# Performance work log

Measured on AMD Instinct MI355X. Metric: run time of the kernel, lower is better.

## Reference

```python
import jax, jax.numpy as jnp
import numpy as np

Q = 9          # D2Q9
G = 8          # dihedral group of the square
X = YD = 768   # spatial grid
HID = 32       # tau_net hidden width
N_IN = 6       # moments with order <= 2 (indices 0..5, contiguous by construction)
LOWER_TAU = 0.8


def _build_stencil():
    # D2Q9 velocities and weights
    e = np.array([[0, 0], [1, 0], [0, 1], [-1, 0], [0, -1],
                  [1, 1], [-1, 1], [-1, -1], [1, -1]], dtype=np.float64)
    w = np.array([4 / 9] + [1 / 9] * 4 + [1 / 36] * 4, dtype=np.float64)
    # natural moment matrix: rows are monomials ex^px * ey^py, ordered so that
    # moment_order = [0,1,1,2,2,2,3,3,4]  ->  in_indices=[0..5], out_indices=[6,7,8]
    exps = [(0, 0), (1, 0), (0, 1), (2, 0), (1, 1), (0, 2), (2, 1), (1, 2), (2, 2)]
    M = np.stack([e[:, 0] ** px * e[:, 1] ** py for px, py in exps])  # [Q, Q]
    Minv = np.linalg.inv(M)
    # symmetry group of the square: 4 rotations x {id, x-axis reflection}
    rots = [np.array([[np.cos(a), -np.sin(a)], [np.sin(a), np.cos(a)]])
            for a in (0.0, np.pi / 2, np.pi, 3 * np.pi / 2)]
    refl = np.array([[1.0, 0.0], [0.0, -1.0]])
    Rs = rots + [r @ refl for r in rots]
    perms = []
    for R in Rs:
        Re = np.rint(e @ R.T)
        P = np.zeros((Q, Q))
        for i in range(Q):
            j = int(np.where((e == Re[i]).all(axis=1))[0][0])
            P[j, i] = 1.0  # velocity i maps to velocity j under R
        perms.append(P)
    P = np.stack(perms)                                   # [G, Q, Q]
    actions = np.einsum('qp,gpr,rs->gqs', M, P, Minv)      # moment action  M P M^-1
    Pt = P.transpose(0, 2, 1)                              # P^-1 = P^T
    inv_actions = np.einsum('qp,gpr,rs->gqs', M, Pt, Minv)
    return (M.astype(np.float32), Minv.astype(np.float32),
            actions.astype(np.float32), inv_actions.astype(np.float32),
            e.astype(np.float32), w.astype(np.float32))


def setup_inputs() -> dict:
    key = jax.random.key(0)
    kf, k1, k2, k3 = jax.random.split(key, 4)
    M, Minv, actions, inv_actions, e, w = _build_stencil()
    f = jax.random.uniform(kf, (Q, X, YD), dtype=jnp.float32)
    s = 0.1
    return {
        'f': f,
        'M': jnp.asarray(M), 'Minv': jnp.asarray(Minv),
        'actions': jnp.asarray(actions), 'inv_actions': jnp.asarray(inv_actions),
        'e': jnp.asarray(e), 'w': jnp.asarray(w),
        'W1': jax.random.normal(k1, (N_IN, HID), jnp.float32) * s,
        'b1': jnp.zeros((HID,), jnp.float32),
        'W2': jax.random.normal(k2, (HID, HID), jnp.float32) * s,
        'b2': jnp.zeros((HID,), jnp.float32),
        'W3': jax.random.normal(k3, (HID, Q - N_IN), jnp.float32) * s,
        'b3': jnp.zeros((Q - N_IN,), jnp.float32),
    }


def reference(f, M, Minv, actions, inv_actions, e, w, W1, b1, W2, b2, W3, b3):
    # --- moment transform: m = M f, moved to channel-last [X, Y, Q] ---
    m = jnp.einsum('qp,pxy->xyq', M, f)
    # --- equivariant tau net on low-order moments ---
    x_in = m[..., :N_IN]                                   # in_indices = 0..5
    Ainv = inv_actions[:, :N_IN, :N_IN]                    # [G, 6, 6]
    A = actions[:, N_IN:, N_IN:]                           # [G, 3, 3] (out_indices)
    xg = jnp.einsum('gij,xyj->gxyi', Ainv, x_in)           # [G, X, Y, 6]
    h = jax.nn.relu(xg @ W1 + b1)
    h = jax.nn.relu(h @ W2 + b2)
    o = h @ W3 + b3                                        # [G, X, Y, 3]
    out = jnp.einsum('gij,gxyj->xyi', A, o)                # sum over group -> [X, Y, 3]
    tau_hi = 1.5 + jax.nn.elu(out)                         # gt_half: > 0.5
    taus = jnp.full(m.shape, LOWER_TAU, m.dtype).at[..., N_IN:].set(tau_hi)
    # --- equilibrium moments: meq = M feq(rho, u) (quadratic BGK, cs^2=1/3) ---
    rho = m[..., 0:1]                                      # natural moments: m0=rho
    u = m[..., 1:3] / rho                                  # m1,m2 = momentum
    eu = jnp.einsum('qd,xyd->xyq', e, u)
    usq = jnp.sum(u * u, axis=-1, keepdims=True)
    feq = w * rho * (1.0 + 3.0 * eu + 4.5 * eu * eu - 1.5 * usq)
    meq = jnp.einsum('qp,xyp->xyq', M, feq)
    # --- MRT collision + inverse transform ---
    m_post = m - (m - meq) / taus
    return jnp.einsum('pq,xyq->pxy', Minv, m_post)
```

## Files before the change

### kernel.cpp

```cpp
#include <hip/hip_runtime.h>
#include <hip/hip_bf16.h>
#include <math.h>

#define Q 9
#define NPIX (768 * 768)

typedef short bf16x8 __attribute__((ext_vector_type(8)));
typedef short s16x2 __attribute__((ext_vector_type(2)));
typedef float f32x4 __attribute__((ext_vector_type(4)));
typedef int i32x4 __attribute__((ext_vector_type(4)));

#define A1BV 512
#define A3V  1024
#define A2V  1536
#define B3TF 6656

__device__ __forceinline__ unsigned short f2bf(float x) {
    unsigned u = __builtin_bit_cast(unsigned, x);
    unsigned r = u + 0x7FFFu + ((u >> 16) & 1u);
    return (unsigned short)(r >> 16);
}

__device__ __forceinline__ unsigned pk2(float e, float o) {
    __hip_bfloat162 h = __float22bfloat162_rn(make_float2(e, o));
    unsigned u;
    __builtin_memcpy(&u, &h, 4);
    return u;
}

__device__ __forceinline__ unsigned relu2(unsigned d) {
    s16x2 v = __builtin_bit_cast(s16x2, d);
    const s16x2 z = {0, 0};
    v = __builtin_elementwise_max(v, z);
    return __builtin_bit_cast(unsigned, v);
}

__device__ __forceinline__ bf16x8 mk8(unsigned w0, unsigned w1, unsigned w2, unsigned w3) {
    i32x4 t = {(int)w0, (int)w1, (int)w2, (int)w3};
    return __builtin_bit_cast(bf16x8, t);
}

__global__ void prep_kernel(const float* __restrict__ actions,
                            const float* __restrict__ inv_actions,
                            const float* __restrict__ W1,
                            const float* __restrict__ b1,
                            const float* __restrict__ W2,
                            const float* __restrict__ W3,
                            const float* __restrict__ b3,
                            short* __restrict__ wsb,
                            float* __restrict__ wsf) {
    const int idx = blockIdx.x * 256 + threadIdx.x;
    if (idx < 8192) {
        int j = idx & 7, l = (idx >> 3) & 63, g = (idx >> 9) & 7, half = idx >> 12;
        int m = l & 15, quad = l >> 4, k = quad * 8 + j;
        int feat = 8 * (m >> 2) + (m & 3) + 4 * half;
        float v = 0.f;
        if (k < 6) {
            #pragma unroll
            for (int i = 0; i < 6; i++)
                v += inv_actions[g * 81 + i * 9 + k] * W1[i * 32 + feat];
        } else if (k == 6) v = b1[feat];
        wsb[idx] = (short)f2bf(v);
    } else if (idx < 12288) {
        int t = idx - 8192;
        int j = t & 7, l = (t >> 3) & 63, g = t >> 9;
        int m = l & 15, quad = l >> 4, k = quad * 8 + j;
        float v = 0.f;
        if (m < 3) {
            #pragma unroll
            for (int j3 = 0; j3 < 3; j3++)
                v += W3[k * 3 + j3] * actions[g * 81 + (6 + m) * 9 + (6 + j3)];
        }
        wsb[idx] = (short)f2bf(v);
    } else if (idx < 13312) {
        int t = idx - 12288;
        int j = t & 7, l = (t >> 3) & 63, half = t >> 9;
        int m = l & 15, quad = l >> 4, k = quad * 8 + j;
        int feat = 8 * (m >> 2) + (m & 3) + 4 * half;
        wsb[idx] = (short)f2bf(W2[k * 32 + feat]);
    } else if (idx < 13315) {
        int t = idx - 13312;
        float acc = 0.f;
        for (int g = 0; g < 8; g++)
            #pragma unroll
            for (int j = 0; j < 3; j++)
                acc += actions[g * 81 + (6 + t) * 9 + (6 + j)] * b3[j];
        wsf[B3TF + t] = acc;
    }
}

__global__ __launch_bounds__(256, 4) void lbm_kernel(
    const float* __restrict__ f,
    const float* __restrict__ Minv,
    const float* __restrict__ w,
    const float* __restrict__ b2,
    const short* __restrict__ wsb,
    const float* __restrict__ wsf,
    float* __restrict__ out) {
    __shared__ float oL[4][64][4];
    (void)Minv;
    (void)w;

    const int tid = threadIdx.x;
    const int wv = tid >> 6;
    const int l = tid & 63;
    const int quad = l >> 4;
    const int lc = l & 15;
    const int p = blockIdx.x * 256 + tid;

    float fv0 = f[0 * NPIX + p], fv1 = f[1 * NPIX + p], fv2 = f[2 * NPIX + p];
    float fv3 = f[3 * NPIX + p], fv4 = f[4 * NPIX + p], fv5 = f[5 * NPIX + p];
    float fv6 = f[6 * NPIX + p], fv7 = f[7 * NPIX + p], fv8 = f[8 * NPIX + p];
    float sa = fv5 + fv6, sb = fv7 + fv8, sc = fv5 - fv6, sd = fv7 - fv8;
    float sab = sa + sb;
    float m4 = sc + sd;
    float p13 = fv1 + fv3, d13 = fv1 - fv3, p24 = fv2 + fv4, d24 = fv2 - fv4;
    float m0 = fv0 + p13 + p24 + sab;
    float m1 = d13 + (sc - sd);
    float m2 = d24 + (sa - sb);
    float m3 = p13 + sab;
    float m5 = p24 + sab;

    unsigned mp0 = pk2(m0, m1), mp1 = pk2(m2, m3), mp2 = pk2(m4, m5);
    const unsigned CONE = 0x00003F80u;
    bf16x8 B1[4];
    #pragma unroll
    for (int nb = 0; nb < 4; nb++) {
        int src = ((nb << 4) | lc) << 2;
        unsigned a = (unsigned)__builtin_amdgcn_ds_bpermute(src, (int)mp0);
        unsigned b = (unsigned)__builtin_amdgcn_ds_bpermute(src, (int)mp1);
        unsigned c = (unsigned)__builtin_amdgcn_ds_bpermute(src, (int)mp2);
        B1[nb] = mk8(a, b, c, CONE);
    }

    const bf16x8* wsv = (const bf16x8*)wsb;
    bf16x8 a2a = wsv[A2V + l], a2b = wsv[A2V + 64 + l];
    f32x4 c2iA = *(const f32x4*)(b2 + 8 * quad);
    f32x4 c2iB = *(const f32x4*)(b2 + 8 * quad + 4);
    float b30 = wsf[B3TF + 0], b31 = wsf[B3TF + 1], b32 = wsf[B3TF + 2];
    f32x4 oinit;
    oinit[0] = (quad == 0) ? b30 : 0.f;
    oinit[1] = (quad == 0) ? b31 : 0.f;
    oinit[2] = (quad == 0) ? b32 : 0.f;
    oinit[3] = 0.f;
    f32x4 oacc[4] = {oinit, oinit, oinit, oinit};

    bf16x8 a1a = wsv[l], a1b = wsv[A1BV + l], a3 = wsv[A3V + l];

    #pragma unroll 1
    for (int g = 0; g < 8; g++) {
        const int gn = (g + 1) & 7;
        bf16x8 na1a = wsv[gn * 64 + l];
        bf16x8 na1b = wsv[A1BV + gn * 64 + l];
        bf16x8 na3  = wsv[A3V + gn * 64 + l];
        #pragma unroll
        for (int nb = 0; nb < 4; nb++) {
            f32x4 z = {0.f, 0.f, 0.f, 0.f};
            f32x4 c1a = __builtin_amdgcn_mfma_f32_16x16x32_bf16(a1a, B1[nb], z, 0, 0, 0);
            f32x4 c1b = __builtin_amdgcn_mfma_f32_16x16x32_bf16(a1b, B1[nb], z, 0, 0, 0);
            bf16x8 B2 = mk8(
                relu2(pk2(c1a[0], c1a[1])),
                relu2(pk2(c1a[2], c1a[3])),
                relu2(pk2(c1b[0], c1b[1])),
                relu2(pk2(c1b[2], c1b[3])));
            f32x4 c2a = __builtin_amdgcn_mfma_f32_16x16x32_bf16(a2a, B2, c2iA, 0, 0, 0);
            f32x4 c2b = __builtin_amdgcn_mfma_f32_16x16x32_bf16(a2b, B2, c2iB, 0, 0, 0);
            bf16x8 B3 = mk8(
                relu2(pk2(c2a[0], c2a[1])),
                relu2(pk2(c2a[2], c2a[3])),
                relu2(pk2(c2b[0], c2b[1])),
                relu2(pk2(c2b[2], c2b[3])));
            oacc[nb] = __builtin_amdgcn_mfma_f32_16x16x32_bf16(a3, B3, oacc[nb], 0, 0, 0);
        }
        a1a = na1a; a1b = na1b; a3 = na3;
    }

    if (quad == 0) {
        #pragma unroll
        for (int nb = 0; nb < 4; nb++)
            *(f32x4*)&oL[wv][nb * 16 + lc][0] = oacc[nb];
    }
    f32x4 ov = *(const f32x4*)&oL[wv][l][0];

    int p2 = p;
    asm("" : "+v"(p2));
    float fr0 = f[0 * NPIX + p2], fr1 = f[1 * NPIX + p2], fr2 = f[2 * NPIX + p2];
    float fr3 = f[3 * NPIX + p2], fr4 = f[4 * NPIX + p2], fr5 = f[5 * NPIX + p2];
    float fr6 = f[6 * NPIX + p2], fr7 = f[7 * NPIX + p2], fr8 = f[8 * NPIX + p2];

    float tinv[3];
    #pragma unroll
    for (int i = 0; i < 3; i++) {
        float o = ov[i];
        float el = (o > 0.f) ? o : (__expf(o) - 1.f);
        tinv[i] = __builtin_amdgcn_rcpf(1.5f + el);
    }

    float rho = m0;
    float ir = __builtin_amdgcn_rcpf(rho);
    float ux = m1 * ir, uy = m2 * ir;
    float usq = ux * ux + uy * uy;
    float base = 1.f - 1.5f * usq;
    float w1r = rho * (1.f / 9.f), w5r = rho * (1.f / 36.f);
    float bx = 3.f * ux, ax = fmaf(4.5f * ux, ux, base);
    float feq1 = w1r * (ax + bx), feq3 = w1r * (ax - bx);
    float by = 3.f * uy, ay = fmaf(4.5f * uy, uy, base);
    float feq2 = w1r * (ay + by), feq4 = w1r * (ay - by);
    float ss = ux + uy, bs = 3.f * ss, as_ = fmaf(4.5f * ss, ss, base);
    float feq5 = w5r * (as_ + bs), feq7 = w5r * (as_ - bs);
    float dd = uy - ux, bd = 3.f * dd, ad = fmaf(4.5f * dd, dd, base);
    float feq6 = w5r * (ad + bd), feq8 = w5r * (ad - bd);

    float g1 = fr1 - feq1, g2 = fr2 - feq2, g3 = fr3 - feq3, g4 = fr4 - feq4;
    float g5 = fr5 - feq5, g6 = fr6 - feq6, g7 = fr7 - feq7, g8 = fr8 - feq8;
    float pa = g1 + g3, pb = g2 + g4;
    float ea = g5 + g6, eb = g7 + g8, ec = g5 - g6, ed = g7 - g8;
    float eab = ea + eb;
    float m3p = pa + eab, m5p = pb + eab, m8p = eab;
    float m6p = ea - eb, m4p = ec + ed, m7p = ec - ed;

    float d3 = 1.25f * m3p, h3 = 0.625f * m3p;
    float d5 = 1.25f * m5p, h5 = 0.625f * m5p;
    float k4 = 0.3125f * m4p;
    float h6 = (0.5f * tinv[0]) * m6p, k6 = 0.5f * h6;
    float h7 = (0.5f * tinv[1]) * m7p, k7 = 0.5f * h7;
    float d8 = tinv[2] * m8p, h8 = 0.5f * d8, k8 = 0.5f * h8;

    float c0 = d8 - d3 - d5;
    float c1 = h3 - h7 - h8;
    float c2 = h5 - h6 - h8;
    float c3 = h3 + h7 - h8;
    float c4 = h5 + h6 - h8;
    float sA = k4 + k7, sB = k6 + k8, sC = k4 + k8;
    float sD = k6 + k7, sE = k7 + k8, sF = k4 + k6;
    float c5 = sA + sB, c6 = sB - sA, c7 = sC - sD, c8 = sE - sF;

    __builtin_nontemporal_store(fr0 - c0, &out[0 * NPIX + p]);
    __builtin_nontemporal_store(fr1 - c1, &out[1 * NPIX + p]);
    __builtin_nontemporal_store(fr2 - c2, &out[2 * NPIX + p]);
    __builtin_nontemporal_store(fr3 - c3, &out[3 * NPIX + p]);
    __builtin_nontemporal_store(fr4 - c4, &out[4 * NPIX + p]);
    __builtin_nontemporal_store(fr5 - c5, &out[5 * NPIX + p]);
    __builtin_nontemporal_store(fr6 - c6, &out[6 * NPIX + p]);
    __builtin_nontemporal_store(fr7 - c7, &out[7 * NPIX + p]);
    __builtin_nontemporal_store(fr8 - c8, &out[8 * NPIX + p]);
}

extern "C" void kernel_launch(void* const* d_in, const int* in_sizes, int n_in,
                              void* d_out, int out_size, void* d_ws, size_t ws_size,
                              hipStream_t stream) {
    const float* f           = (const float*)d_in[0];
    const float* Minv        = (const float*)d_in[2];
    const float* actions     = (const float*)d_in[3];
    const float* inv_actions = (const float*)d_in[4];
    const float* w           = (const float*)d_in[6];
    const float* W1          = (const float*)d_in[7];
    const float* b1          = (const float*)d_in[8];
    const float* W2          = (const float*)d_in[9];
    const float* b2          = (const float*)d_in[10];
    const float* W3          = (const float*)d_in[11];
    const float* b3          = (const float*)d_in[12];
    float* outp = (float*)d_out;
    short* wsb = (short*)d_ws;
    float* wsf = (float*)d_ws;

    prep_kernel<<<53, 256, 0, stream>>>(actions, inv_actions, W1, b1, W2, W3, b3, wsb, wsf);
    lbm_kernel<<<NPIX / 256, 256, 0, stream>>>(f, Minv, w, b2, wsb, wsf, outp);
}
```

Measured before the change: 121.1 us.

## Switch MLP to 32x32x16 MFMA tiles and peel last group iteration

Rewrites the per-group MLP to use 32x32x16 bf16 MFMAs over 32-pixel tiles instead of 16x16x32 over 16-pixel blocks. The weights are repacked in the prep kernel with a hidden-unit permutation so the MFMA output layout feeds directly into the next layer's B operand. This cuts the instruction count and the bpermute shuffles. The final group iteration is peeled so the reload of f overlaps with MFMA work. Occupancy is lowered to 3 blocks per SM to make room for the larger accumulators, which risks reduced latency hiding.

New measurement: 119.5 us. Within noise of the previous version (-1.3%).

```diff
diff --git a/kernel.cpp b/kernel.cpp
--- a/kernel.cpp
+++ b/kernel.cpp
@@ -8,12 +8,18 @@
 typedef short bf16x8 __attribute__((ext_vector_type(8)));
 typedef short s16x2 __attribute__((ext_vector_type(2)));
 typedef float f32x4 __attribute__((ext_vector_type(4)));
+typedef float f32x16 __attribute__((ext_vector_type(16)));
 typedef int i32x4 __attribute__((ext_vector_type(4)));
 
-#define A1BV 512
-#define A3V  1024
-#define A2V  1536
-#define B3TF 6656
+#define A3LOV 512
+#define A3HIV 1024
+#define A2LOV 1536
+#define A2HIV 1600
+#define B3TF  6656
+
+__device__ __forceinline__ int hidmap(int k) {
+    return (k & 3) + 8 * ((k >> 2) & 1) + 4 * (k >> 3);
+}
 
 __device__ __forceinline__ unsigned short f2bf(float x) {
     unsigned u = __builtin_bit_cast(unsigned, x);
@@ -50,34 +56,48 @@
                             short* __restrict__ wsb,
                             float* __restrict__ wsf) {
     const int idx = blockIdx.x * 256 + threadIdx.x;
-    if (idx < 8192) {
-        int j = idx & 7, l = (idx >> 3) & 63, g = (idx >> 9) & 7, half = idx >> 12;
-        int m = l & 15, quad = l >> 4, k = quad * 8 + j;
-        int feat = 8 * (m >> 2) + (m & 3) + 4 * half;
+    if (idx < 4096) {
+        int j = idx & 7, l = (idx >> 3) & 63, g = idx >> 9;
+        int m = l & 31, k = (l >> 5) * 8 + j;
         float v = 0.f;
         if (k < 6) {
             #pragma unroll
             for (int i = 0; i < 6; i++)
-                v += inv_actions[g * 81 + i * 9 + k] * W1[i * 32 + feat];
-        } else if (k == 6) v = b1[feat];
+                v += inv_actions[g * 81 + i * 9 + k] * W1[i * 32 + m];
+        } else if (k == 6) v = b1[m];
+        wsb[idx] = (short)f2bf(v);
+    } else if (idx < 8192) {
+        int t = idx - 4096;
+        int j = t & 7, l = (t >> 3) & 63, g = t >> 9;
+        int m = l & 31, kk = (l >> 5) * 8 + j, h = hidmap(kk);
+        float v = 0.f;
+        if (m < 3) {
+            #pragma unroll
+            for (int j3 = 0; j3 < 3; j3++)
+                v += W3[h * 3 + j3] * actions[g * 81 + (6 + m) * 9 + (6 + j3)];
+        }
         wsb[idx] = (short)f2bf(v);
     } else if (idx < 12288) {
         int t = idx - 8192;
         int j = t & 7, l = (t >> 3) & 63, g = t >> 9;
-        int m = l & 15, quad = l >> 4, k = quad * 8 + j;
+        int m = l & 31, kk = (l >> 5) * 8 + j, h = 16 + hidmap(kk);
         float v = 0.f;
         if (m < 3) {
             #pragma unroll
             for (int j3 = 0; j3 < 3; j3++)
-                v += W3[k * 3 + j3] * actions[g * 81 + (6 + m) * 9 + (6 + j3)];
+                v += W3[h * 3 + j3] * actions[g * 81 + (6 + m) * 9 + (6 + j3)];
         }
         wsb[idx] = (short)f2bf(v);
+    } else if (idx < 12800) {
+        int t = idx - 12288;
+        int j = t & 7, l = (t >> 3) & 63;
+        int m = l & 31, kk = (l >> 5) * 8 + j;
+        wsb[idx] = (short)f2bf(W2[hidmap(kk) * 32 + m]);
     } else if (idx < 13312) {
-        int t = idx - 12288;
-        int j = t & 7, l = (t >> 3) & 63, half = t >> 9;
-        int m = l & 15, quad = l >> 4, k = quad * 8 + j;
-        int feat = 8 * (m >> 2) + (m & 3) + 4 * half;
-        wsb[idx] = (short)f2bf(W2[k * 32 + feat]);
+        int t = idx - 12800;
+        int j = t & 7, l = (t >> 3) & 63;
+        int m = l & 31, kk = (l >> 5) * 8 + j;
+        wsb[idx] = (short)f2bf(W2[(16 + hidmap(kk)) * 32 + m]);
     } else if (idx < 13315) {
         int t = idx - 13312;
         float acc = 0.f;
@@ -89,7 +109,24 @@
     }
 }
 
-__global__ __launch_bounds__(256, 4) void lbm_kernel(
+#define MLP_BODY(WA1, W3LO, W3HI, B1F, OACC)                                          \
+    {                                                                                 \
+        f32x16 C1 = __builtin_amdgcn_mfma_f32_32x32x16_bf16(WA1, B1F, z16, 0, 0, 0);  \
+        bf16x8 B2lo = mk8(relu2(pk2(C1[0], C1[1])), relu2(pk2(C1[2], C1[3])),         \
+                          relu2(pk2(C1[4], C1[5])), relu2(pk2(C1[6], C1[7])));        \
+        bf16x8 B2hi = mk8(relu2(pk2(C1[8], C1[9])), relu2(pk2(C1[10], C1[11])),       \
+                          relu2(pk2(C1[12], C1[13])), relu2(pk2(C1[14], C1[15])));    \
+        f32x16 C2 = __builtin_amdgcn_mfma_f32_32x32x16_bf16(a2hi, B2hi, c2i, 0, 0, 0);\
+        C2 = __builtin_amdgcn_mfma_f32_32x32x16_bf16(a2lo, B2lo, C2, 0, 0, 0);        \
+        bf16x8 B3lo = mk8(relu2(pk2(C2[0], C2[1])), relu2(pk2(C2[2], C2[3])),         \
+                          relu2(pk2(C2[4], C2[5])), relu2(pk2(C2[6], C2[7])));        \
+        bf16x8 B3hi = mk8(relu2(pk2(C2[8], C2[9])), relu2(pk2(C2[10], C2[11])),       \
+                          relu2(pk2(C2[12], C2[13])), relu2(pk2(C2[14], C2[15])));    \
+        OACC = __builtin_amdgcn_mfma_f32_32x32x16_bf16(W3HI, B3hi, OACC, 0, 0, 0);    \
+        OACC = __builtin_amdgcn_mfma_f32_32x32x16_bf16(W3LO, B3lo, OACC, 0, 0, 0);    \
+    }
+
+__global__ __launch_bounds__(256, 3) void lbm_kernel(
     const float* __restrict__ f,
     const float* __restrict__ Minv,
     const float* __restrict__ w,
@@ -104,8 +141,7 @@
     const int tid = threadIdx.x;
     const int wv = tid >> 6;
     const int l = tid & 63;
-    const int quad = l >> 4;
-    const int lc = l & 15;
+    const int hi = l >> 5;
     const int p = blockIdx.x * 256 + tid;
 
     float fv0 = f[0 * NPIX + p], fv1 = f[1 * NPIX + p], fv2 = f[2 * NPIX + p];
@@ -123,70 +159,61 @@
 
     unsigned mp0 = pk2(m0, m1), mp1 = pk2(m2, m3), mp2 = pk2(m4, m5);
     const unsigned CONE = 0x00003F80u;
-    bf16x8 B1[4];
-    #pragma unroll
-    for (int nb = 0; nb < 4; nb++) {
-        int src = ((nb << 4) | lc) << 2;
-        unsigned a = (unsigned)__builtin_amdgcn_ds_bpermute(src, (int)mp0);
-        unsigned b = (unsigned)__builtin_amdgcn_ds_bpermute(src, (int)mp1);
-        unsigned c = (unsigned)__builtin_amdgcn_ds_bpermute(src, (int)mp2);
-        B1[nb] = mk8(a, b, c, CONE);
-    }
+    const int s0 = (l & 31) << 2;
+    const int s1 = s0 | (32 << 2);
+    bf16x8 B1A = mk8((unsigned)__builtin_amdgcn_ds_bpermute(s0, (int)mp0),
+                     (unsigned)__builtin_amdgcn_ds_bpermute(s0, (int)mp1),
+                     (unsigned)__builtin_amdgcn_ds_bpermute(s0, (int)mp2), CONE);
+    bf16x8 B1B = mk8((unsigned)__builtin_amdgcn_ds_bpermute(s1, (int)mp0),
+                     (unsigned)__builtin_amdgcn_ds_bpermute(s1, (int)mp1),
+                     (unsigned)__builtin_amdgcn_ds_bpermute(s1, (int)mp2), CONE);
 
     const bf16x8* wsv = (const bf16x8*)wsb;
-    bf16x8 a2a = wsv[A2V + l], a2b = wsv[A2V + 64 + l];
-    f32x4 c2iA = *(const f32x4*)(b2 + 8 * quad);
-    f32x4 c2iB = *(const f32x4*)(b2 + 8 * quad + 4);
+    bf16x8 a2lo = wsv[A2LOV + l], a2hi = wsv[A2HIV + l];
+    f32x16 c2i;
+    #pragma unroll
+    for (int r = 0; r < 16; r++) {
+        const int base = (r & 3) + 8 * (r >> 2);
+        c2i[r] = hi ? b2[base + 4] : b2[base];
+    }
     float b30 = wsf[B3TF + 0], b31 = wsf[B3TF + 1], b32 = wsf[B3TF + 2];
-    f32x4 oinit;
-    oinit[0] = (quad == 0) ? b30 : 0.f;
-    oinit[1] = (quad == 0) ? b31 : 0.f;
-    oinit[2] = (quad == 0) ? b32 : 0.f;
-    oinit[3] = 0.f;
-    f32x4 oacc[4] = {oinit, oinit, oinit, oinit};
-
-    bf16x8 a1a = wsv[l], a1b = wsv[A1BV + l], a3 = wsv[A3V + l];
-
+    f32x16 oinit;
+    #pragma unroll
+    for (int r = 0; r < 16; r++) oinit[r] = 0.f;
+    oinit[0] = hi ? 0.f : b30;
+    oinit[1] = hi ? 0.f : b31;
+    oinit[2] = hi ? 0.f : b32;
+    f32x16 oaccA = oinit, oaccB = oinit;
+    f32x16 z16;
+    #pragma unroll
+    for (int r = 0; r < 16; r++) z16[r] = 0.f;
+
+    bf16x8 wa1 = wsv[l], w3lo = wsv[A3LOV + l], w3hi = wsv[A3HIV + l];
     #pragma unroll 1
-    for (int g = 0; g < 8; g++) {
-        const int gn = (g + 1) & 7;
-        bf16x8 na1a = wsv[gn * 64 + l];
-        bf16x8 na1b = wsv[A1BV + gn * 64 + l];
-        bf16x8 na3  = wsv[A3V + gn * 64 + l];
-        #pragma unroll
-        for (int nb = 0; nb < 4; nb++) {
-            f32x4 z = {0.f, 0.f, 0.f, 0.f};
-            f32x4 c1a = __builtin_amdgcn_mfma_f32_16x16x32_bf16(a1a, B1[nb], z, 0, 0, 0);
-            f32x4 c1b = __builtin_amdgcn_mfma_f32_16x16x32_bf16(a1b, B1[nb], z, 0, 0, 0);
-            bf16x8 B2 = mk8(
-                relu2(pk2(c1a[0], c1a[1])),
-                relu2(pk2(c1a[2], c1a[3])),
-                relu2(pk2(c1b[0], c1b[1])),
-                relu2(pk2(c1b[2], c1b[3])));
-            f32x4 c2a = __builtin_amdgcn_mfma_f32_16x16x32_bf16(a2a, B2, c2iA, 0, 0, 0);
-            f32x4 c2b = __builtin_amdgcn_mfma_f32_16x16x32_bf16(a2b, B2, c2iB, 0, 0, 0);
-            bf16x8 B3 = mk8(
-                relu2(pk2(c2a[0], c2a[1])),
-                relu2(pk2(c2a[2], c2a[3])),
-                relu2(pk2(c2b[0], c2b[1])),
-                relu2(pk2(c2b[2], c2b[3])));
-            oacc[nb] = __builtin_amdgcn_mfma_f32_16x16x32_bf16(a3, B3, oacc[nb], 0, 0, 0);
-        }
-        a1a = na1a; a1b = na1b; a3 = na3;
-    }
-
-    if (quad == 0) {
-        #pragma unroll
-        for (int nb = 0; nb < 4; nb++)
-            *(f32x4*)&oL[wv][nb * 16 + lc][0] = oacc[nb];
-    }
-    f32x4 ov = *(const f32x4*)&oL[wv][l][0];
-
+    for (int g = 0; g < 7; g++) {
+        const int gn = g + 1;
+        bf16x8 na1  = wsv[gn * 64 + l];
+        bf16x8 n3lo = wsv[A3LOV + gn * 64 + l];
+        bf16x8 n3hi = wsv[A3HIV + gn * 64 + l];
+        MLP_BODY(wa1, w3lo, w3hi, B1A, oaccA);
+        MLP_BODY(wa1, w3lo, w3hi, B1B, oaccB);
+        wa1 = na1; w3lo = n3lo; w3hi = n3hi;
+    }
     int p2 = p;
     asm("" : "+v"(p2));
     float fr0 = f[0 * NPIX + p2], fr1 = f[1 * NPIX + p2], fr2 = f[2 * NPIX + p2];
     float fr3 = f[3 * NPIX + p2], fr4 = f[4 * NPIX + p2], fr5 = f[5 * NPIX + p2];
     float fr6 = f[6 * NPIX + p2], fr7 = f[7 * NPIX + p2], fr8 = f[8 * NPIX + p2];
+    MLP_BODY(wa1, w3lo, w3hi, B1A, oaccA);
+    MLP_BODY(wa1, w3lo, w3hi, B1B, oaccB);
+
+    if (hi == 0) {
+        f32x4 t0 = {oaccA[0], oaccA[1], oaccA[2], oaccA[3]};
+        *(f32x4*)&oL[wv][l & 31][0] = t0;
+        f32x4 t1 = {oaccB[0], oaccB[1], oaccB[2], oaccB[3]};
+        *(f32x4*)&oL[wv][32 + (l & 31)][0] = t1;
+    }
+    f32x4 ov = *(const f32x4*)&oL[wv][l][0];
 
     float tinv[3];
     #pragma unroll
@@ -254,8 +281,8 @@
     const float* actions     = (const float*)d_in[3];
     const float* inv_actions = (const float*)d_in[4];
     const float* w           = (const float*)d_in[6];
+    const float* b1          = (const float*)d_in[8];
     const float* W1          = (const float*)d_in[7];
-    const float* b1          = (const float*)d_in[8];
     const float* W2          = (const float*)d_in[9];
     const float* b2          = (const float*)d_in[10];
     const float* W3          = (const float*)d_in[11];
```
